# Optimization experiments

Hardware: AMD Instinct MI355X
Metric: run time of the kernel (lower is better)

## Reference

```python
import jax, jax.numpy as jnp
import numpy as np
import math

B, S, D = 2, 2048, 2048
H, HK = 32, 8          # query heads, kv heads
HD = D // H            # 64
REP = H // HK          # 4


def setup_inputs() -> dict:
    key = jax.random.key(0)
    ks = jax.random.split(key, 6)
    x = jax.random.normal(ks[0], (B, S, D), jnp.float32)
    # RoPE tables, rotate_half convention: halves duplicated along last dim
    inv_freq = 1.0 / (10000.0 ** (jnp.arange(0, HD, 2, dtype=jnp.float32) / HD))
    freqs = jnp.arange(S, dtype=jnp.float32)[:, None] * inv_freq[None, :]  # [S, HD/2]
    cos = jnp.concatenate([jnp.cos(freqs), jnp.cos(freqs)], axis=-1)       # [S, HD]
    sin = jnp.concatenate([jnp.sin(freqs), jnp.sin(freqs)], axis=-1)
    attn_mask = jnp.tril(jnp.ones((S, S), dtype=bool))
    std = 1.0 / math.sqrt(D)
    wq = jax.random.normal(ks[1], (D, D), jnp.float32) * std
    wk = jax.random.normal(ks[2], (HK * HD, D), jnp.float32) * std
    wv = jax.random.normal(ks[3], (HK * HD, D), jnp.float32) * std
    wo = jax.random.normal(ks[4], (D, D), jnp.float32) * std
    return {"x": x, "cos": cos, "sin": sin, "attn_mask": attn_mask,
            "wq": wq, "wk": wk, "wv": wv, "wo": wo}


def _rotate_half(t):
    h = t.shape[-1] // 2
    return jnp.concatenate([-t[..., h:], t[..., :h]], axis=-1)


def reference(x, cos, sin, attn_mask, wq, wk, wv, wo):
    b, s, d = x.shape
    q = (x @ wq.T).reshape(b, s, H, HD).transpose(0, 2, 1, 3)    # [b,H,s,hd]
    k = (x @ wk.T).reshape(b, s, HK, HD).transpose(0, 2, 1, 3)   # [b,HK,s,hd]
    v = (x @ wv.T).reshape(b, s, HK, HD).transpose(0, 2, 1, 3)
    c = cos[:s][None, None]
    sn = sin[:s][None, None]
    q = q * c + _rotate_half(q) * sn
    k = k * c + _rotate_half(k) * sn
    # GQA: group query heads instead of repeat_interleave'ing KV
    # repeat_interleave order == reshape (HK, REP): heads [g*REP : (g+1)*REP] share kv group g
    qg = q.reshape(b, HK, REP, s, HD)
    scores = jnp.einsum('bgrsd,bgtd->bgrst', qg, k) / math.sqrt(HD)  # [b,HK,REP,s,s]
    m = attn_mask[None, None, None, :, :]
    scores = jnp.where(m, scores, -jnp.inf)
    attn = jax.nn.softmax(scores, axis=-1)
    out = jnp.einsum('bgrst,bgtd->bgrsd', attn, v)                  # [b,HK,REP,s,hd]
    out = out.reshape(b, H, s, HD).transpose(0, 2, 1, 3).reshape(b, s, d)
    return out @ wo.T
```

## Files before the change

kernel.cpp:

```cpp
#include <hip/hip_runtime.h>
#include <hip/hip_bf16.h>
#include <math.h>

typedef __hip_bfloat16 bf16;
typedef __attribute__((ext_vector_type(8))) short bf16x8;
typedef __attribute__((ext_vector_type(4))) short short4v;
typedef __attribute__((ext_vector_type(4))) float f32x4;
typedef __attribute__((ext_vector_type(4))) unsigned int u32x4;

static constexpr int B = 2, S = 2048, D = 2048, H = 32, HK = 8, HD = 64;
static constexpr int M = B * S;
static constexpr int NKV = HK * HD;
static constexpr int QKV3 = D + 2 * NKV;
static constexpr float SCALE2 = 0.125f * 1.44269504f;

__device__ __forceinline__ short bfbits(float x) {
  bf16 h = __float2bfloat16(x);
  return *reinterpret_cast<short*>(&h);
}

__device__ __forceinline__ float bf2f(short bits) {
  unsigned int u = ((unsigned int)(unsigned short)bits) << 16;
  return __builtin_bit_cast(float, u);
}

__device__ __forceinline__ void gl_lds16(const bf16* gp, bf16* lp) {
  __builtin_amdgcn_global_load_lds(
      (const __attribute__((address_space(1))) unsigned int*)(const void*)gp,
      (__attribute__((address_space(3))) unsigned int*)(void*)lp, 16, 0, 0);
}

struct alignas(8) bf4 { bf16 v[4]; };
static constexpr int N4_X  = M * D / 4;
static constexpr int N4_WQ = D * D / 4;
static constexpr int N4_WK = NKV * D / 4;
static constexpr int E0 = N4_X;
static constexpr int E1 = E0 + N4_WQ;
static constexpr int E2 = E1 + N4_WK;
static constexpr int E3 = E2 + N4_WK;
static constexpr int E4 = E3 + N4_WQ;
__global__ __launch_bounds__(256) void cast_all_kernel(const float* __restrict__ x,
                                                       const float* __restrict__ wq,
                                                       const float* __restrict__ wk,
                                                       const float* __restrict__ wv,
                                                       const float* __restrict__ wo,
                                                       bf16* __restrict__ xb,
                                                       bf16* __restrict__ wqkv,
                                                       bf16* __restrict__ wob) {
  int i = blockIdx.x * 256 + threadIdx.x;
  int stride = gridDim.x * 256;
  for (; i < E4; i += stride) {
    const float* s; bf16* d; int j;
    if (i < E0)      { s = x;  d = xb;   j = i; }
    else if (i < E1) { s = wq; d = wqkv; j = i - E0; }
    else if (i < E2) { s = wk; d = wqkv + (size_t)N4_WQ * 4; j = i - E1; }
    else if (i < E3) { s = wv; d = wqkv + (size_t)(N4_WQ + N4_WK) * 4; j = i - E2; }
    else             { s = wo; d = wob;  j = i - E3; }
    float4 f = reinterpret_cast<const float4*>(s)[j];
    bf4 o;
    o.v[0] = __float2bfloat16(f.x);
    o.v[1] = __float2bfloat16(f.y);
    o.v[2] = __float2bfloat16(f.z);
    o.v[3] = __float2bfloat16(f.w);
    reinterpret_cast<bf4*>(d)[j] = o;
  }
}

__global__ __launch_bounds__(512, 1) void gemm256_kernel(const bf16* __restrict__ A,
                                                         const bf16* __restrict__ Bt,
                                                         bf16* __restrict__ C,
                                                         int Ndim, int Kdim) {
  __shared__ __align__(16) bf16 As[2][256 * 64];
  __shared__ __align__(16) bf16 Bs[2][256 * 64];
  const int tid = threadIdx.x;
  const int wv = tid >> 6;
  const int wm = wv >> 2, wn = wv & 3;
  const int lane = tid & 63;
  const int r16 = lane & 15, g = lane >> 4;

  const int nwg = gridDim.x;
  const int lin = blockIdx.x;
  const int swz = (lin & 7) * (nwg >> 3) + (lin >> 3);
  const int gx = Ndim >> 8;
  const int bn = swz % gx;
  const int bm = swz / gx;

  f32x4 acc[8][4] = {};
  const int nk = Kdim >> 6;

  auto stage = [&](int buf, int t) {
#pragma unroll
    for (int i = 0; i < 4; ++i) {
      int u = tid + i * 512;
      int rr = u >> 3, c8 = u & 7;
      int c8s = c8 ^ (rr & 7);
      gl_lds16(&A[(size_t)(bm * 256 + rr) * Kdim + t * 64 + c8s * 8], &As[buf][0] + (size_t)u * 8);
    }
#pragma unroll
    for (int i = 0; i < 4; ++i) {
      int u = tid + i * 512;
      int rr = u >> 3, c8 = u & 7;
      int c8s = c8 ^ (rr & 7);
      gl_lds16(&Bt[(size_t)(bn * 256 + rr) * Kdim + t * 64 + c8s * 8], &Bs[buf][0] + (size_t)u * 8);
    }
  };

  auto gtile = [&](int CUR, int t) {
    if (t + 1 < nk) asm volatile("s_waitcnt vmcnt(16)" ::: "memory");
    else            asm volatile("s_waitcnt vmcnt(0)" ::: "memory");
    __builtin_amdgcn_sched_barrier(0);
    __builtin_amdgcn_s_barrier();
    __builtin_amdgcn_sched_barrier(0);
    __builtin_amdgcn_s_setprio(1);
#pragma unroll
    for (int kc = 0; kc < 2; ++kc) {
      bf16x8 af[8], bfr[4];
      const int kq = kc * 4 + g;
#pragma unroll
      for (int m = 0; m < 8; ++m) {
        int ra = wm * 128 + m * 16 + r16;
        af[m] = *reinterpret_cast<const bf16x8*>(&As[CUR][(size_t)ra * 64 + ((kq ^ (ra & 7)) * 8)]);
      }
#pragma unroll
      for (int n = 0; n < 4; ++n) {
        int rb = wn * 64 + n * 16 + r16;
        bfr[n] = *reinterpret_cast<const bf16x8*>(&Bs[CUR][(size_t)rb * 64 + ((kq ^ (rb & 7)) * 8)]);
      }
#pragma unroll
      for (int m = 0; m < 8; ++m)
#pragma unroll
        for (int n = 0; n < 4; ++n)
          acc[m][n] = __builtin_amdgcn_mfma_f32_16x16x32_bf16(af[m], bfr[n], acc[m][n], 0, 0, 0);
    }
    __builtin_amdgcn_s_setprio(0);
    asm volatile("s_waitcnt lgkmcnt(0)" ::: "memory");
    __builtin_amdgcn_sched_barrier(0);
    __builtin_amdgcn_s_barrier();
    __builtin_amdgcn_sched_barrier(0);
    if (t + 2 < nk) stage(CUR, t + 2);
  };

  stage(0, 0);
  stage(1, 1);
  for (int t = 0; t < nk; t += 2) {
    gtile(0, t);
    gtile(1, t + 1);
  }

  const int row0 = bm * 256 + wm * 128 + g * 4;
  const int col0 = bn * 256 + wn * 64 + r16;
#pragma unroll
  for (int m = 0; m < 8; ++m)
#pragma unroll
    for (int n = 0; n < 4; ++n)
#pragma unroll
      for (int j = 0; j < 4; ++j)
        C[(size_t)(row0 + m * 16 + j) * Ndim + col0 + n * 16] = __float2bfloat16(acc[m][n][j]);
}

template <bool OUT_F32>
__global__ __launch_bounds__(256) void gemm_bt_kernel(const bf16* __restrict__ A,
                                                      const bf16* __restrict__ Bt,
                                                      void* __restrict__ C,
                                                      int Ndim, int Kdim) {
  __shared__ __align__(16) bf16 As[128][64];
  __shared__ __align__(16) bf16 Bs[128][64];
  const int tid = threadIdx.x;
  const int lane = tid & 63;
  const int w = tid >> 6;
  const int wm = w >> 1, wn = w & 1;
  const int r16 = lane & 15, g = lane >> 4;
  const int bm = blockIdx.y, bn = blockIdx.x;
  f32x4 acc[4][4] = {};

  const int nk = Kdim >> 6;
  for (int kt = 0; kt < nk; ++kt) {
    __syncthreads();
#pragma unroll
    for (int i = 0; i < 4; ++i) {
      int u = tid + i * 256;
      int rr = u >> 3, c8 = u & 7;
      int c8s = c8 ^ (rr & 7);
      gl_lds16(&A[(size_t)(bm * 128 + rr) * Kdim + kt * 64 + c8s * 8], &As[0][0] + (size_t)u * 8);
      gl_lds16(&Bt[(size_t)(bn * 128 + rr) * Kdim + kt * 64 + c8s * 8], &Bs[0][0] + (size_t)u * 8);
    }
    __syncthreads();
#pragma unroll
    for (int kc = 0; kc < 2; ++kc) {
      bf16x8 af[4], bfr[4];
      const int kq = kc * 4 + g;
#pragma unroll
      for (int m = 0; m < 4; ++m) {
        int ra = wm * 64 + m * 16 + r16;
        af[m] = *reinterpret_cast<const bf16x8*>(&As[ra][(kq ^ (ra & 7)) * 8]);
        int rb = wn * 64 + m * 16 + r16;
        bfr[m] = *reinterpret_cast<const bf16x8*>(&Bs[rb][(kq ^ (rb & 7)) * 8]);
      }
#pragma unroll
      for (int m = 0; m < 4; ++m)
#pragma unroll
        for (int n = 0; n < 4; ++n)
          acc[m][n] = __builtin_amdgcn_mfma_f32_16x16x32_bf16(af[m], bfr[n], acc[m][n], 0, 0, 0);
    }
  }
  const int row0 = bm * 128 + wm * 64 + g * 4;
  const int col0 = bn * 128 + wn * 64 + r16;
#pragma unroll
  for (int m = 0; m < 4; ++m)
#pragma unroll
    for (int n = 0; n < 4; ++n)
#pragma unroll
      for (int j = 0; j < 4; ++j) {
        size_t idx = (size_t)(row0 + m * 16 + j) * Ndim + col0 + n * 16;
        if (OUT_F32)
          reinterpret_cast<float*>(C)[idx] = acc[m][n][j];
        else
          reinterpret_cast<bf16*>(C)[idx] = __float2bfloat16(acc[m][n][j]);
      }
}

__global__ __launch_bounds__(256) void rope_k_kernel(bf16* __restrict__ t,
                                                     const float* __restrict__ cosb,
                                                     const float* __restrict__ sinb) {
  int idx = blockIdx.x * 256 + threadIdx.x;
  int i = idx & 31;
  int rest = idx >> 5;
  int hh = rest & 7;
  int s = (rest >> 3) % S;
  int b = rest / (8 * S);
  size_t base = ((size_t)b * S + s) * QKV3 + D + hh * HD;
  float x0 = __bfloat162float(t[base + i]);
  float x1 = __bfloat162float(t[base + i + 32]);
  float c = cosb[s * HD + i];
  float sn = sinb[s * HD + i];
  t[base + i] = __float2bfloat16(x0 * c - x1 * sn);
  t[base + i + 32] = __float2bfloat16(x1 * c + x0 * sn);
}

__global__ __launch_bounds__(256) void transpose_v_kernel(const bf16* __restrict__ qkv,
                                                          bf16* __restrict__ vt) {
  __shared__ bf16 tile[64][65];
  const int st = blockIdx.x;
  const int bk = blockIdx.y;
  const int b = bk >> 3, hk = bk & 7;
  const int tid = threadIdx.x;
#pragma unroll
  for (int i = 0; i < 16; ++i) {
    int idx = tid + i * 256;
    int rs = idx >> 6, c = idx & 63;
    tile[rs][c] = qkv[((size_t)b * S + st * 64 + rs) * QKV3 + (D + NKV) + hk * HD + c];
  }
  __syncthreads();
#pragma unroll
  for (int i = 0; i < 16; ++i) {
    int idx = tid + i * 256;
    int rh = idx >> 6, cs = idx & 63;
    int blk = cs >> 5, kvl = cs & 31;
    int pos = ((kvl >> 2) & 3) * 8 + ((kvl >> 4) << 2) + (kvl & 3);
    vt[(((size_t)b * HK + hk) * HD + rh) * S + st * 64 + blk * 32 + pos] = tile[cs][rh];
  }
}

__global__ __launch_bounds__(256, 2) void attn_kernel(const bf16* __restrict__ qkv,
                                                      const bf16* __restrict__ vt,
                                                      const float* __restrict__ cosb,
                                                      const float* __restrict__ sinb,
                                                      bf16* __restrict__ ao) {
  __shared__ __align__(16) bf16 Ksh[2][64 * 64];
  __shared__ __align__(16) bf16 Vsh[2][64 * 64];
  const int u = blockIdx.x;
  const int y = blockIdx.y;
  const int b = y >> 3, hk = y & 7;
  const int tid = threadIdx.x;
  const int w = tid >> 6;
  const int h = hk * 4 + w;
  const int lane = tid & 63;
  const int r = lane & 15, g = lane >> 4;

  const bf16* qp  = qkv + ((size_t)b * S) * QKV3 + h * HD;
  const bf16* kvp = qkv + ((size_t)b * S) * QKV3 + D + hk * HD;
  const bf16* vtp = vt + (((size_t)b * HK + hk) * HD) * S;
  const int srow = tid >> 3;
  const int sc8 = tid & 7;

  bf16x8 ones;
#pragma unroll
  for (int j = 0; j < 8; ++j) ones[j] = (short)0x3F80;

  auto stage64 = [&](int buf, int kv0) {
#pragma unroll
    for (int i = 0; i < 2; ++i) {
      int rr = srow + i * 32;
      int cs = sc8 ^ (rr & 7);
      gl_lds16(&kvp[(size_t)(kv0 + rr) * QKV3 + cs * 8], &Ksh[buf][((size_t)rr * 8 + sc8) * 8]);
    }
#pragma unroll
    for (int i = 0; i < 2; ++i) {
      int rr = srow + i * 32;
      int cs = sc8 ^ (rr & 7);
      gl_lds16(&vtp[(size_t)rr * S + kv0 + cs * 8], &Vsh[buf][((size_t)rr * 8 + sc8) * 8]);
    }
  };

  for (int pass = 0; pass < 2; ++pass) {
    const int qb = pass ? (2016 - u * 32) : (u * 32);
    bf16x8 qfr[2][2];
#pragma unroll
    for (int qq = 0; qq < 2; ++qq) {
      const int srowq = qb + qq * 16 + r;
      bf16x8 f0 = *reinterpret_cast<const bf16x8*>(&qp[(size_t)srowq * QKV3 + g * 8]);
      bf16x8 f1 = *reinterpret_cast<const bf16x8*>(&qp[(size_t)srowq * QKV3 + 32 + g * 8]);
      float4 c0 = reinterpret_cast<const float4*>(&cosb[(size_t)srowq * HD + g * 8])[0];
      float4 c1 = reinterpret_cast<const float4*>(&cosb[(size_t)srowq * HD + g * 8])[1];
      float4 s0 = reinterpret_cast<const float4*>(&sinb[(size_t)srowq * HD + g * 8])[0];
      float4 s1 = reinterpret_cast<const float4*>(&sinb[(size_t)srowq * HD + g * 8])[1];
      float cc[8] = {c0.x, c0.y, c0.z, c0.w, c1.x, c1.y, c1.z, c1.w};
      float ss[8] = {s0.x, s0.y, s0.z, s0.w, s1.x, s1.y, s1.z, s1.w};
#pragma unroll
      for (int j = 0; j < 8; ++j) {
        float x0 = bf2f(f0[j]), x1 = bf2f(f1[j]);
        qfr[qq][0][j] = bfbits((x0 * cc[j] - x1 * ss[j]) * SCALE2);
        qfr[qq][1][j] = bfbits((x1 * cc[j] + x0 * ss[j]) * SCALE2);
      }
    }

    f32x4 o[4][2] = {};
    f32x4 ol[2] = {};
    const int kv_end = qb + 32;
    const int nch = (kv_end + 63) >> 6;

    auto chunk = [&](int CUR, int cc, bool lastc) {
      const int kv0 = cc * 64;
      if (!lastc) stage64(CUR ^ 1, kv0 + 64);
      f32x4 scv[4][2] = {};
      __builtin_amdgcn_s_setprio(1);
#pragma unroll
      for (int f = 0; f < 4; ++f) {
        const int row = f * 16 + r;
#pragma unroll
        for (int hc = 0; hc < 2; ++hc) {
          bf16x8 kf = *reinterpret_cast<const bf16x8*>(
              &Ksh[CUR][(size_t)row * 64 + (((hc * 4 + g) ^ (r & 7)) * 8)]);
          scv[f][0] = __builtin_amdgcn_mfma_f32_16x16x32_bf16(kf, qfr[0][hc], scv[f][0], 0, 0, 0);
          scv[f][1] = __builtin_amdgcn_mfma_f32_16x16x32_bf16(kf, qfr[1][hc], scv[f][1], 0, 0, 0);
        }
      }
      __builtin_amdgcn_s_setprio(0);
      if (lastc) {
#pragma unroll
        for (int qq = 0; qq < 2; ++qq) {
          const int lim = qb + qq * 16 + r - kv0;
#pragma unroll
          for (int f = 0; f < 4; ++f)
#pragma unroll
            for (int j = 0; j < 4; ++j)
              if (f * 16 + g * 4 + j > lim) scv[f][qq][j] = -1e30f;
        }
      }
#pragma unroll
      for (int blk = 0; blk < 2; ++blk) {
        u32x4 pk0, pk1;
#pragma unroll
        for (int pj = 0; pj < 4; ++pj) {
          const int f = blk * 2 + (pj >> 1);
          const int j0 = (pj & 1) * 2;
          float a0 = __builtin_amdgcn_exp2f(scv[f][0][j0]);
          float a1 = __builtin_amdgcn_exp2f(scv[f][0][j0 + 1]);
          pk0[pj] = (__builtin_bit_cast(unsigned int, a0) >> 16) |
                    (__builtin_bit_cast(unsigned int, a1) & 0xffff0000u);
          float b0 = __builtin_amdgcn_exp2f(scv[f][1][j0]);
          float b1 = __builtin_amdgcn_exp2f(scv[f][1][j0 + 1]);
          pk1[pj] = (__builtin_bit_cast(unsigned int, b0) >> 16) |
                    (__builtin_bit_cast(unsigned int, b1) & 0xffff0000u);
        }
        bf16x8 pb0 = __builtin_bit_cast(bf16x8, pk0);
        bf16x8 pb1 = __builtin_bit_cast(bf16x8, pk1);
        __builtin_amdgcn_s_setprio(1);
        ol[0] = __builtin_amdgcn_mfma_f32_16x16x32_bf16(ones, pb0, ol[0], 0, 0, 0);
        ol[1] = __builtin_amdgcn_mfma_f32_16x16x32_bf16(ones, pb1, ol[1], 0, 0, 0);
#pragma unroll
        for (int d = 0; d < 4; ++d) {
          bf16x8 vf = *reinterpret_cast<const bf16x8*>(
              &Vsh[CUR][(size_t)(d * 16 + r) * 64 + (((blk * 4 + g) ^ (r & 7)) * 8)]);
          o[d][0] = __builtin_amdgcn_mfma_f32_16x16x32_bf16(vf, pb0, o[d][0], 0, 0, 0);
          o[d][1] = __builtin_amdgcn_mfma_f32_16x16x32_bf16(vf, pb1, o[d][1], 0, 0, 0);
        }
        __builtin_amdgcn_s_setprio(0);
      }
      __syncthreads();
    };

    stage64(0, 0);
    __syncthreads();
    int c = 0;
    for (; c + 2 <= nch; c += 2) {
      chunk(0, c, c == nch - 1);
      chunk(1, c + 1, c + 1 == nch - 1);
    }
    if (c < nch) chunk(0, c, true);

#pragma unroll
    for (int qq = 0; qq < 2; ++qq) {
      float inv = 1.0f / ol[qq][0];
#pragma unroll
      for (int d = 0; d < 4; ++d) {
        short4v ov;
        ov[0] = bfbits(o[d][qq][0] * inv);
        ov[1] = bfbits(o[d][qq][1] * inv);
        ov[2] = bfbits(o[d][qq][2] * inv);
        ov[3] = bfbits(o[d][qq][3] * inv);
        *reinterpret_cast<short4v*>(
            &ao[(((size_t)b * S + qb + qq * 16 + r) * H + h) * HD + d * 16 + g * 4]) = ov;
      }
    }
  }
}

extern "C" void kernel_launch(void* const* d_in, const int* in_sizes, int n_in,
                              void* d_out, int out_size, void* d_ws, size_t ws_size,
                              hipStream_t stream) {
  (void)in_sizes; (void)n_in; (void)out_size; (void)ws_size;
  const float* x    = (const float*)d_in[0];
  const float* cosb = (const float*)d_in[1];
  const float* sinb = (const float*)d_in[2];
  const float* wq   = (const float*)d_in[4];
  const float* wk   = (const float*)d_in[5];
  const float* wv   = (const float*)d_in[6];
  const float* wo   = (const float*)d_in[7];

  char* ws = (char*)d_ws;
  size_t off = 0;
  auto alloc = [&](size_t elems) {
    bf16* p = (bf16*)(ws + off);
    off = (off + elems * sizeof(bf16) + 255) & ~(size_t)255;
    return p;
  };
  bf16* xb    = alloc((size_t)M * D);
  bf16* wqkvb = alloc((size_t)QKV3 * D);
  bf16* wob   = alloc((size_t)D * D);
  bf16* qkvb  = alloc((size_t)M * QKV3);
  bf16* vtb   = alloc((size_t)B * HK * HD * S);
  bf16* aob   = alloc((size_t)M * D);

  cast_all_kernel<<<dim3(2048), dim3(256), 0, stream>>>(x, wq, wk, wv, wo, xb, wqkvb, wob);

  gemm256_kernel<<<dim3((M / 256) * (QKV3 / 256)), dim3(512), 0, stream>>>(xb, wqkvb, qkvb, QKV3, D);

  rope_k_kernel<<<dim3(B * S * 8 * 32 / 256), 256, 0, stream>>>(qkvb, cosb, sinb);

  transpose_v_kernel<<<dim3(S / 64, B * HK), 256, 0, stream>>>(qkvb, vtb);

  attn_kernel<<<dim3(32, B * HK), 256, 0, stream>>>(qkvb, vtb, cosb, sinb, aob);

  gemm_bt_kernel<true><<<dim3(D / 128, M / 128), 256, 0, stream>>>(aob, wob, d_out, D, D);
}
```

Measured before the change: 184.2 us.

## Restructure 256x256 GEMM into 4-slot K=32 pipeline with interleaved staging

The 256x256 bf16 GEMM moves from a two-buffer pipeline with K=64 tiles to four LDS slots of K=32, prefetching three steps ahead. Each half-step is split into two MFMA phases, and the A and B global-to-LDS loads for a future slot are issued between them, so loads overlap with matrix math. The LDS swizzle is changed to fit the narrower 32-column rows. The cost is more barriers per K step and tighter vmcnt bookkeeping, which could stall if the scheduling is wrong.

```diff
diff --git a/kernel.cpp b/kernel.cpp
--- a/kernel.cpp
+++ b/kernel.cpp
@@ -70,13 +70,13 @@
                                                          const bf16* __restrict__ Bt,
                                                          bf16* __restrict__ C,
                                                          int Ndim, int Kdim) {
-  __shared__ __align__(16) bf16 As[2][256 * 64];
-  __shared__ __align__(16) bf16 Bs[2][256 * 64];
+  __shared__ __align__(16) bf16 As[4][256 * 32];
+  __shared__ __align__(16) bf16 Bs[4][256 * 32];
   const int tid = threadIdx.x;
-  const int wv = tid >> 6;
-  const int wm = wv >> 2, wn = wv & 3;
+  const int wave = tid >> 6;
+  const int wm = wave >> 2, wn = wave & 3;
   const int lane = tid & 63;
-  const int r16 = lane & 15, g = lane >> 4;
+  const int r = lane & 15, g = lane >> 4;
 
   const int nwg = gridDim.x;
   const int lin = blockIdx.x;
@@ -86,69 +86,94 @@
   const int bm = swz / gx;
 
   f32x4 acc[8][4] = {};
-  const int nk = Kdim >> 6;
-
-  auto stage = [&](int buf, int t) {
-#pragma unroll
-    for (int i = 0; i < 4; ++i) {
+  const int nh = Kdim >> 5;
+  const int pchE = (g ^ (r & 3) ^ ((r >> 2) & 3)) * 8;
+
+  auto stageA = [&](int slot, int h) {
+#pragma unroll
+    for (int i = 0; i < 2; ++i) {
       int u = tid + i * 512;
-      int rr = u >> 3, c8 = u & 7;
-      int c8s = c8 ^ (rr & 7);
-      gl_lds16(&A[(size_t)(bm * 256 + rr) * Kdim + t * 64 + c8s * 8], &As[buf][0] + (size_t)u * 8);
-    }
-#pragma unroll
-    for (int i = 0; i < 4; ++i) {
+      int rr = u >> 2, pc = u & 3;
+      int lc = pc ^ (rr & 3) ^ ((rr >> 2) & 3);
+      gl_lds16(&A[(size_t)(bm * 256 + rr) * Kdim + h * 32 + lc * 8],
+               &As[slot][0] + (size_t)u * 8);
+    }
+  };
+  auto stageB = [&](int slot, int h) {
+#pragma unroll
+    for (int i = 0; i < 2; ++i) {
       int u = tid + i * 512;
-      int rr = u >> 3, c8 = u & 7;
-      int c8s = c8 ^ (rr & 7);
-      gl_lds16(&Bt[(size_t)(bn * 256 + rr) * Kdim + t * 64 + c8s * 8], &Bs[buf][0] + (size_t)u * 8);
+      int rr = u >> 2, pc = u & 3;
+      int lc = pc ^ (rr & 3) ^ ((rr >> 2) & 3);
+      gl_lds16(&Bt[(size_t)(bn * 256 + rr) * Kdim + h * 32 + lc * 8],
+               &Bs[slot][0] + (size_t)u * 8);
     }
   };
 
-  auto gtile = [&](int CUR, int t) {
-    if (t + 1 < nk) asm volatile("s_waitcnt vmcnt(16)" ::: "memory");
-    else            asm volatile("s_waitcnt vmcnt(0)" ::: "memory");
+  auto halfstep = [&](int slot, int h) {
+    const int s3 = (slot + 3) & 3;
+    bf16x8 af[8], bfr[4];
+#pragma unroll
+    for (int m = 0; m < 4; ++m)
+      af[m] = *reinterpret_cast<const bf16x8*>(
+          &As[slot][(size_t)(wm * 128 + m * 16 + r) * 32 + pchE]);
+#pragma unroll
+    for (int n = 0; n < 4; ++n)
+      bfr[n] = *reinterpret_cast<const bf16x8*>(
+          &Bs[slot][(size_t)(wn * 64 + n * 16 + r) * 32 + pchE]);
+    if (h + 3 < nh) stageA(s3, h + 3);
     __builtin_amdgcn_sched_barrier(0);
     __builtin_amdgcn_s_barrier();
+    asm volatile("s_waitcnt lgkmcnt(0)" ::: "memory");
     __builtin_amdgcn_sched_barrier(0);
     __builtin_amdgcn_s_setprio(1);
 #pragma unroll
-    for (int kc = 0; kc < 2; ++kc) {
-      bf16x8 af[8], bfr[4];
-      const int kq = kc * 4 + g;
-#pragma unroll
-      for (int m = 0; m < 8; ++m) {
-        int ra = wm * 128 + m * 16 + r16;
-        af[m] = *reinterpret_cast<const bf16x8*>(&As[CUR][(size_t)ra * 64 + ((kq ^ (ra & 7)) * 8)]);
-      }
-#pragma unroll
-      for (int n = 0; n < 4; ++n) {
-        int rb = wn * 64 + n * 16 + r16;
-        bfr[n] = *reinterpret_cast<const bf16x8*>(&Bs[CUR][(size_t)rb * 64 + ((kq ^ (rb & 7)) * 8)]);
-      }
-#pragma unroll
-      for (int m = 0; m < 8; ++m)
-#pragma unroll
-        for (int n = 0; n < 4; ++n)
-          acc[m][n] = __builtin_amdgcn_mfma_f32_16x16x32_bf16(af[m], bfr[n], acc[m][n], 0, 0, 0);
-    }
+    for (int m = 0; m < 4; ++m)
+#pragma unroll
+      for (int n = 0; n < 4; ++n)
+        acc[m][n] = __builtin_amdgcn_mfma_f32_16x16x32_bf16(af[m], bfr[n], acc[m][n], 0, 0, 0);
     __builtin_amdgcn_s_setprio(0);
+    __builtin_amdgcn_sched_barrier(0);
+    __builtin_amdgcn_s_barrier();
+#pragma unroll
+    for (int m = 4; m < 8; ++m)
+      af[m] = *reinterpret_cast<const bf16x8*>(
+          &As[slot][(size_t)(wm * 128 + m * 16 + r) * 32 + pchE]);
+    if (h + 3 < nh) stageB(s3, h + 3);
+    __builtin_amdgcn_sched_barrier(0);
+    __builtin_amdgcn_s_barrier();
     asm volatile("s_waitcnt lgkmcnt(0)" ::: "memory");
     __builtin_amdgcn_sched_barrier(0);
+    __builtin_amdgcn_s_setprio(1);
+#pragma unroll
+    for (int m = 4; m < 8; ++m)
+#pragma unroll
+      for (int n = 0; n < 4; ++n)
+        acc[m][n] = __builtin_amdgcn_mfma_f32_16x16x32_bf16(af[m], bfr[n], acc[m][n], 0, 0, 0);
+    __builtin_amdgcn_s_setprio(0);
+    if (h + 3 < nh)      asm volatile("s_waitcnt vmcnt(8)" ::: "memory");
+    else if (h + 2 < nh) asm volatile("s_waitcnt vmcnt(4)" ::: "memory");
+    else if (h + 1 < nh) asm volatile("s_waitcnt vmcnt(0)" ::: "memory");
+    __builtin_amdgcn_sched_barrier(0);
     __builtin_amdgcn_s_barrier();
-    __builtin_amdgcn_sched_barrier(0);
-    if (t + 2 < nk) stage(CUR, t + 2);
   };
 
-  stage(0, 0);
-  stage(1, 1);
-  for (int t = 0; t < nk; t += 2) {
-    gtile(0, t);
-    gtile(1, t + 1);
+  stageA(0, 0); stageB(0, 0);
+  stageA(1, 1); stageB(1, 1);
+  stageA(2, 2); stageB(2, 2);
+  asm volatile("s_waitcnt vmcnt(8)" ::: "memory");
+  __builtin_amdgcn_sched_barrier(0);
+  __builtin_amdgcn_s_barrier();
+
+  for (int h = 0; h < nh; h += 4) {
+    halfstep(0, h);
+    halfstep(1, h + 1);
+    halfstep(2, h + 2);
+    halfstep(3, h + 3);
   }
 
   const int row0 = bm * 256 + wm * 128 + g * 4;
-  const int col0 = bn * 256 + wn * 64 + r16;
+  const int col0 = bn * 256 + wn * 64 + r;
 #pragma unroll
   for (int m = 0; m < 8; ++m)
 #pragma unroll
```

Result: no change. 185.4 us (+0.6%).
